# Kernel tuning notes

Measured on AMD Instinct MI355X. Metric: run time of the kernel, lower is better.

## Reference

```python
import jax, jax.numpy as jnp
import numpy as np

V = 50257
VPAD = 50304
D = 768
H = 6
HD = 128
L = 12
T = 2048
BLOCK = 128
NB = T // BLOCK
EPS = 1.1920929e-07  # torch.finfo(float32).eps, F.rms_norm default
ATTN_SCALE = 0.12


def rms_norm(x):
    return x * jax.lax.rsqrt(jnp.mean(jnp.square(x), axis=-1, keepdims=True) + EPS)


def rotary_tables(t):
    af = (1.0 / 1024) ** jnp.linspace(0.0, 1.0, HD // 4)
    af = jnp.concatenate([af, jnp.zeros(HD // 4)])  # half of HD/2 freqs are zero
    theta = jnp.arange(t, dtype=jnp.float32)[:, None] * af[None, :]  # [T, HD/2]
    return jnp.cos(theta), jnp.sin(theta)


def apply_rotary(x, cos, sin):
    # x: [B,T,H,HD]
    x1, x2 = jnp.split(x, 2, axis=-1)
    c = cos[None, :, None, :]
    s = sin[None, :, None, :]
    return jnp.concatenate([x1 * c + x2 * s, -x1 * s + x2 * c], axis=-1)


def build_elem_masks(input_seq, sw_long):
    # Reproduces create_block_masks: block-sparse document-causal + sliding window.
    docs = jnp.cumsum((input_seq == 50256).astype(jnp.int32))
    bi = jnp.arange(NB)
    docs_b = docs.reshape(NB, BLOCK)
    dlo, dhi = docs_b[:, 0], docs_b[:, -1]
    any_bm = (bi[:, None] >= bi[None, :]) & (dlo[:, None] <= dhi[None, :]) & (dhi[:, None] >= dlo[None, :])
    all_bm = (bi[:, None] > bi[None, :]) & (dlo[:, None] == dhi[None, :]) & (dhi[:, None] == dlo[None, :])
    partial_bm = any_bm & (~all_bm)

    def rank_desc(m):
        # rank of each True block among that row's True blocks ordered by descending kv index
        mi = m.astype(jnp.int32)
        return jnp.cumsum(mi[:, ::-1], axis=1)[:, ::-1] - mi

    pr = rank_desc(partial_bm)
    fr = rank_desc(all_bm)
    full_cnt = jnp.sum(all_bm.astype(jnp.int32), axis=1)
    ti = jnp.arange(T)
    causal_e = ti[:, None] >= ti[None, :]
    doc_e = docs[:, None] == docs[None, :]

    def bm(sw):
        # BlockMask.from_kv_blocks keeps nearest blocks:
        # partial kept count = min(partial_cnt, max(sw - full_cnt, 1)); full kept count = min(full_cnt, sw - 1)
        keep_p = partial_bm & (pr < jnp.maximum(sw - full_cnt, 1)[:, None])
        keep_f = all_bm & (fr < (sw - 1))
        kp = jnp.repeat(jnp.repeat(keep_p, BLOCK, axis=0), BLOCK, axis=1)
        kf = jnp.repeat(jnp.repeat(keep_f, BLOCK, axis=0), BLOCK, axis=1)
        # full blocks skip mask_mod; partial blocks apply elementwise document_causal
        return kf | (kp & causal_e & doc_e)

    return bm(sw_long), bm(sw_long // 2)


def attention(x, ve, qkv_w, lam, proj_w, cos, sin, mask):
    B = x.shape[0]
    qkv = jnp.einsum('btd,fd->btf', x, qkv_w.reshape(3 * H * HD, D))
    q, k, v = [a.reshape(B, T, H, HD) for a in jnp.split(qkv, 3, axis=-1)]
    q = apply_rotary(rms_norm(q), cos, sin)
    k = apply_rotary(rms_norm(k), cos, sin)
    if ve is not None:
        v = lam[0] * v + lam[1] * ve.reshape(v.shape)
    else:
        v = lam[0] * v
    scores = jnp.einsum('bthd,bshd->bhts', q, k) * ATTN_SCALE
    scores = jnp.where(mask[None, None], scores, -jnp.inf)
    p = jax.nn.softmax(scores, axis=-1)
    y = jnp.einsum('bhts,bshd->bthd', p, v).reshape(B, T, H * HD)
    return y @ proj_w.T


def mlp(x, fc_w, proj_w):
    h = x @ fc_w.T
    return jnp.square(jax.nn.relu(h)) @ proj_w.T


def forward(input_seq, target_seq, sw, embed_w, ve_w, qkv_w, attn_lambdas, attn_proj_w,
            mlp_fc_w, mlp_proj_w, block_lambdas, skip_weights, lm_head_w):
    long_m, short_m = build_elem_masks(input_seq, sw)
    cos, sin = rotary_tables(T)
    x = x0 = rms_norm(embed_w[input_seq][None])  # [1,T,D]
    ve0, ve1, ve2 = ve_w[0][input_seq], ve_w[1][input_seq], ve_w[2][input_seq]
    ve = [ve0, ve1, ve2, None, None, None, None, None, None, ve0, ve1, ve2]
    enc_masks = [long_m, short_m, short_m, short_m, long_m, short_m]
    masks = enc_masks + enc_masks[::-1]
    skips = []
    for i in range(6):  # encoder
        x = block_lambdas[i, 0] * x + block_lambdas[i, 1] * x0
        x = x + attention(rms_norm(x), ve[i], qkv_w[i], attn_lambdas[i], attn_proj_w[i], cos, sin, masks[i])
        x = x + mlp(rms_norm(x), mlp_fc_w[i], mlp_proj_w[i])
        skips.append(x)
    for j in range(6):  # decoder with U-net skips
        i = 6 + j
        x = x + skip_weights[j] * skips.pop()
        x = block_lambdas[i, 0] * x + block_lambdas[i, 1] * x0
        if i != 7:  # layer 7 has no attention
            x = x + attention(rms_norm(x), ve[i], qkv_w[i], attn_lambdas[i], attn_proj_w[i], cos, sin, masks[i])
        x = x + mlp(rms_norm(x), mlp_fc_w[i], mlp_proj_w[i])
    x = rms_norm(x)
    logits = (x @ lm_head_w.T).astype(jnp.float32)
    logits = 30.0 * jax.nn.sigmoid(logits / (7.5 * (D ** 0.5)))
    logp = jax.nn.log_softmax(logits.reshape(T, VPAD), axis=-1)
    return -jnp.mean(jnp.take_along_axis(logp, target_seq[:, None], axis=1))


def setup_inputs():
    key = jax.random.key(0)
    ks = jax.random.split(key, 10)

    def rn(k, shape, std):
        return jax.random.normal(k, shape, dtype=jnp.float32) * std

    s_d = 0.5 / (D ** 0.5)
    s_h = 0.5 / ((4 * D) ** 0.5)
    input_seq = jax.random.randint(ks[0], (T,), 0, V)
    input_seq = input_seq.at[jnp.arange(0, T, 512)].set(50256)  # doc separators
    return {
        'input_seq': input_seq,
        'target_seq': jax.random.randint(ks[1], (T,), 0, V),
        'sliding_window_num_blocks': 8,
        'embed_w': rn(ks[2], (V, D), 0.02),
        've_w': rn(ks[3], (3, V, D), 0.02),
        'qkv_w': rn(ks[4], (L, 3, H * HD, D), s_d),
        'attn_lambdas': jnp.tile(jnp.array([0.5, 0.5], dtype=jnp.float32), (L, 1)),
        'attn_proj_w': rn(ks[5], (L, D, H * HD), s_d),
        'mlp_fc_w': rn(ks[6], (L, 4 * D, D), s_d),
        'mlp_proj_w': rn(ks[7], (L, D, 4 * D), s_h),
        'block_lambdas': jnp.tile(jnp.array([1.0, 0.0], dtype=jnp.float32), (L, 1)),
        'skip_weights': jnp.ones((6,), dtype=jnp.float32),
        'lm_head_w': rn(ks[8], (VPAD, D), 0.005),
    }


def reference(input_seq, target_seq, sliding_window_num_blocks, embed_w, ve_w, qkv_w,
              attn_lambdas, attn_proj_w, mlp_fc_w, mlp_proj_w, block_lambdas,
              skip_weights, lm_head_w):
    return forward(input_seq, target_seq, sliding_window_num_blocks, embed_w, ve_w, qkv_w,
                   attn_lambdas, attn_proj_w, mlp_fc_w, mlp_proj_w, block_lambdas,
                   skip_weights, lm_head_w)
```

## Files before the change

### kernel.cpp

```cpp
#include <hip/hip_runtime.h>
#include <hip/hip_bf16.h>

#define TT 2048
#define DD 768
#define HH 6
#define HDIM 128
#define NL 12
#define NBL 16
#define BLKSZ 128
#define DFF 3072
#define VP 50304
#define NV 50257
#define EPSF 1.1920929e-07f

typedef unsigned short u16;
typedef __attribute__((ext_vector_type(8))) short short8v;
typedef __attribute__((ext_vector_type(4))) float f32x4;
typedef __attribute__((address_space(3))) void lds_void;
typedef __attribute__((address_space(1))) void gbl_void;

__device__ __forceinline__ u16 f2bf(float f){
  unsigned u = __float_as_uint(f);
  return (u16)((u + 0x7fffu + ((u >> 16) & 1u)) >> 16);
}
__device__ __forceinline__ float bf2f(u16 u){
  return __uint_as_float((unsigned)u << 16);
}
__device__ __forceinline__ void async16(const void* g, void* l){
  __builtin_amdgcn_global_load_lds((const gbl_void*)g, (lds_void*)l, 16, 0, 0);
}

__device__ __forceinline__ float wave_sum(float v){
#pragma unroll
  for (int o = 32; o > 0; o >>= 1) v += __shfl_xor(v, o);
  return v;
}
__device__ __forceinline__ float block_sum(float v){
  __shared__ float sh[9];
  int lane = threadIdx.x & 63, w = threadIdx.x >> 6;
  v = wave_sum(v);
  if (lane == 0) sh[w] = v;
  __syncthreads();
  if (threadIdx.x == 0){
    float tot = 0.f;
    int nw = (blockDim.x + 63) >> 6;
    for (int i = 0; i < nw; i++) tot += sh[i];
    sh[8] = tot;
  }
  __syncthreads();
  return sh[8];
}

__global__ void k_f2bf_all(const float* __restrict__ qkvw, const float* __restrict__ aproj,
                           const float* __restrict__ fcw, const float* __restrict__ mproj,
                           const float* __restrict__ lmw,
                           u16* __restrict__ qkvw_bf, u16* __restrict__ aprojw_bf,
                           u16* __restrict__ fcw_bf, u16* __restrict__ mprojw_bf,
                           u16* __restrict__ lmw_bf){
  const long S0 = 2654208;
  const long S1 = S0 + 884736;
  const long S2 = S1 + 3538944;
  const long S3 = S2 + 3538944;
  const long S4 = S3 + 4829184;
  long stride = (long)gridDim.x * blockDim.x;
  for (long g = (long)blockIdx.x * blockDim.x + threadIdx.x; g < S4; g += stride){
    const float* in; u16* out; long off;
    if (g < S0){ in = qkvw;  out = qkvw_bf;  off = g; }
    else if (g < S1){ in = aproj; out = aprojw_bf; off = g - S0; }
    else if (g < S2){ in = fcw;   out = fcw_bf;   off = g - S1; }
    else if (g < S3){ in = mproj; out = mprojw_bf; off = g - S2; }
    else { in = lmw; out = lmw_bf; off = g - S3; }
    const float4* p = (const float4*)(in + off * 8);
    float4 a = p[0], b = p[1];
    u16 o[8] = { f2bf(a.x), f2bf(a.y), f2bf(a.z), f2bf(a.w),
                 f2bf(b.x), f2bf(b.y), f2bf(b.z), f2bf(b.w) };
    *(ulonglong2*)(out + off * 8) = *(const ulonglong2*)o;
  }
}

__global__ void k_docs_masks(const int* __restrict__ seq, const int* __restrict__ swnb,
                             int* __restrict__ docs, int* __restrict__ bmask){
  if (threadIdx.x != 0) return;
  int c = 0;
  for (int t = 0; t < TT; t++){ c += (seq[t] == 50256); docs[t] = c; }
  int dlo[NBL], dhi[NBL];
  for (int b = 0; b < NBL; b++){ dlo[b] = docs[b*BLKSZ]; dhi[b] = docs[b*BLKSZ + BLKSZ-1]; }
  int allb[NBL][NBL], partb[NBL][NBL];
  for (int i = 0; i < NBL; i++)
    for (int j = 0; j < NBL; j++){
      int a = (i >= j) && (dlo[i] <= dhi[j]) && (dhi[i] >= dlo[j]);
      int f = (i >  j) && (dlo[i] == dhi[j]) && (dhi[i] == dlo[j]);
      allb[i][j] = f; partb[i][j] = a && !f;
    }
  int sws[2]; sws[0] = swnb[0]; sws[1] = swnb[0] / 2;
  for (int m = 0; m < 2; m++){
    int sw = sws[m];
    for (int i = 0; i < NBL; i++){
      int fullcnt = 0;
      for (int j = 0; j < NBL; j++) fullcnt += allb[i][j];
      int pth = sw - fullcnt; if (pth < 1) pth = 1;
      int pr = 0, fr = 0;
      for (int j = NBL-1; j >= 0; j--){
        int kp = partb[i][j] && (pr < pth);
        int kf = allb[i][j]  && (fr < sw - 1);
        bmask[(m*2+0)*NBL*NBL + i*NBL + j] = kf;
        bmask[(m*2+1)*NBL*NBL + i*NBL + j] = kp;
        pr += partb[i][j]; fr += allb[i][j];
      }
    }
  }
}

__global__ void k_embed(const int* __restrict__ seq, const float* __restrict__ embw,
                        const float* __restrict__ vew, float* __restrict__ x,
                        float* __restrict__ x0, u16* __restrict__ veg,
                        float* __restrict__ cosb, float* __restrict__ sinb){
  int t = blockIdx.x;
  if (threadIdx.x < 64){
    int j = threadIdx.x;
    float c = 1.f, s = 0.f;
    if (j < 32){
      float af = powf(1.0f/1024.0f, (float)j / 31.0f);
      float th = (float)t * af;
      c = cosf(th); s = sinf(th);
    }
    cosb[t*64 + j] = c; sinb[t*64 + j] = s;
  }
  int tok = seq[t];
  const float* row = embw + (size_t)tok * DD;
  float ss = 0.f;
  for (int d = threadIdx.x; d < DD; d += blockDim.x){ float v = row[d]; ss += v*v; }
  float tot = block_sum(ss);
  float rn = rsqrtf(tot / DD + EPSF);
  for (int d = threadIdx.x; d < DD; d += blockDim.x){
    float v = row[d] * rn;
    x[(size_t)t*DD + d] = v; x0[(size_t)t*DD + d] = v;
  }
  for (int j = 0; j < 3; j++){
    const float* vr = vew + ((size_t)j*NV + tok) * DD;
    u16* dst = veg + ((size_t)j*TT + t) * DD;
    for (int d = threadIdx.x; d < DD; d += blockDim.x) dst[d] = f2bf(vr[d]);
  }
}

__global__ void k_rmsnorm_bf(const float* __restrict__ in, u16* __restrict__ out,
                             float* __restrict__ rowsum){
  int t = blockIdx.x;
  if (rowsum && threadIdx.x == 0) rowsum[t] = 0.f;
  const float* r = in + (size_t)t * DD;
  float ss = 0.f;
  for (int d = threadIdx.x; d < DD; d += blockDim.x){ float v = r[d]; ss += v*v; }
  float tot = block_sum(ss);
  float rn = rsqrtf(tot / DD + EPSF);
  u16* o = out + (size_t)t * DD;
  for (int d = threadIdx.x; d < DD; d += blockDim.x) o[d] = f2bf(r[d] * rn);
}

__global__ void k_premix_norm(float* __restrict__ x, const float* __restrict__ x0,
                              const float* __restrict__ sk, float* __restrict__ sk_out,
                              const float* __restrict__ skw, int j,
                              const float* __restrict__ bl, int layer, u16* __restrict__ xn){
  int t = blockIdx.x;
  float bl0 = bl[layer*2], bl1 = bl[layer*2 + 1];
  float sw = sk ? skw[j] : 0.f;
  float vloc[3];
  float ss = 0.f;
  int base = t * DD;
#pragma unroll
  for (int k = 0; k < 3; k++){
    int d = threadIdx.x + k*256;
    float xin = x[base + d];
    if (sk_out) sk_out[base + d] = xin;
    float v = xin;
    if (sk) v += sw * sk[base + d];
    v = bl0 * v + bl1 * x0[base + d];
    vloc[k] = v; ss += v*v;
  }
  float tot = block_sum(ss);
  float rn = rsqrtf(tot / DD + EPSF);
#pragma unroll
  for (int k = 0; k < 3; k++){
    int d = threadIdx.x + k*256;
    x[base + d] = vloc[k];
    xn[base + d] = f2bf(vloc[k] * rn);
  }
}

template<int MODE, int BN>
__global__ __launch_bounds__(256, 4) void k_mfma_gemm(const u16* __restrict__ A, const u16* __restrict__ B,
                                                   float* __restrict__ C, u16* __restrict__ Cbf,
                                                   const u16* __restrict__ vegp, const float* __restrict__ lam,
                                                   int layer, u16* __restrict__ vtb,
                                                   int N, int K, int ldk, int nbn){
  constexpr int NW  = BN / 32;
  constexpr int BC  = BN / 64 * 2;
  __shared__ u16 As[128*64];
  __shared__ u16 Bs[BN*64];
  int per = (nbn << 4) >> 3;
  int x = (blockIdx.x & 7) * per + (blockIdx.x >> 3);
  int bm = (x & 15) << 7;
  int bn = (x >> 4) * BN;
  int koff = (MODE == 5) ? blockIdx.y * K : 0;
  int tid = threadIdx.x;
  int wid = tid >> 6, lane = tid & 63;
  int wr = wid >> 1, wc = wid & 1;
  int srow = lane >> 3;
  int scol = (((lane & 7) ^ srow) * 8);
  int l15 = lane & 15, l16 = lane >> 4;
  const u16* pa[4];
  const u16* pb[BC];
#pragma unroll
  for (int c = 0; c < 4; c++){
    int row = (wid*4 + c)*8 + srow;
    pa[c] = A + (size_t)(bm + row) * ldk + koff + scol;
  }
#pragma unroll
  for (int c = 0; c < BC; c++){
    int row = (wid*BC + c)*8 + srow;
    pb[c] = B + (size_t)(bn + row) * ldk + koff + scol;
  }
  f32x4 acc[4][NW] = {};
  for (int k0 = 0; k0 < K; k0 += 64){
#pragma unroll
    for (int c = 0; c < 4; c++){
      async16(pa[c], As + (wid*4 + c) * 512);
      pa[c] += 64;
    }
#pragma unroll
    for (int c = 0; c < BC; c++){
      async16(pb[c], Bs + (wid*BC + c) * 512);
      pb[c] += 64;
    }
    __syncthreads();
#pragma unroll
    for (int kk = 0; kk < 2; kk++){
      short8v a[4], b[NW];
#pragma unroll
      for (int m = 0; m < 4; m++){
        int row = wr*64 + m*16 + l15;
        a[m] = *(const short8v*)(As + row*64 + ((((kk<<2)|l16) ^ (row&7))<<3));
      }
#pragma unroll
      for (int n = 0; n < NW; n++){
        int row = wc*(BN/2) + n*16 + l15;
        b[n] = *(const short8v*)(Bs + row*64 + ((((kk<<2)|l16) ^ (row&7))<<3));
      }
#pragma unroll
      for (int m = 0; m < 4; m++)
#pragma unroll
        for (int n = 0; n < NW; n++)
          acc[m][n] = __builtin_amdgcn_mfma_f32_16x16x32_bf16(a[m], b[n], acc[m][n], 0, 0, 0);
    }
    __syncthreads();
  }
  if (MODE == 4 && bn >= 1536){
    int h = (bn - 1536) >> 7;
    int dbase = (bn - 1536) & 127;
    float l0 = lam[layer*2], l1 = lam[layer*2 + 1];
#pragma unroll
    for (int m = 0; m < 4; m++){
      int t0 = bm + wr*64 + m*16 + l16*4;
#pragma unroll
      for (int n = 0; n < NW; n++){
        int d = dbase + wc*(BN/2) + n*16 + l15;
        u16 o[4];
#pragma unroll
        for (int j = 0; j < 4; j++){
          float v = l0 * acc[m][n][j];
          if (vegp) v += l1 * bf2f(vegp[(size_t)(t0 + j)*DD + h*HDIM + d]);
          o[j] = f2bf(v);
        }
        *(ushort4*)(vtb + ((size_t)(h*HDIM + d))*TT + t0) = *(const ushort4*)o;
      }
    }
    return;
  }
#pragma unroll
  for (int m = 0; m < 4; m++){
    int row = bm + wr*64 + m*16 + l16*4;
#pragma unroll
    for (int j = 0; j < 4; j++){
      if (MODE == 3){
        u16* cb = Cbf + (size_t)(row + j) * N + bn + wc*(BN/2) + l15;
#pragma unroll
        for (int n = 0; n < NW; n++){
          float v = fmaxf(acc[m][n][j], 0.f);
          cb[n*16] = f2bf(v * v);
        }
      } else if (MODE == 4){
        u16* cb = Cbf + (size_t)(row + j) * 1536 + bn + wc*(BN/2) + l15;
#pragma unroll
        for (int n = 0; n < NW; n++) cb[n*16] = f2bf(acc[m][n][j]);
      } else if (MODE == 5){
        float* cp = C + (size_t)(row + j) * N + bn + wc*(BN/2) + l15;
#pragma unroll
        for (int n = 0; n < NW; n++) atomicAdd(cp + n*16, acc[m][n][j]);
      } else {
        float* cp = C + (size_t)(row + j) * N + bn + wc*(BN/2) + l15;
#pragma unroll
        for (int n = 0; n < NW; n++) cp[n*16] = acc[m][n][j];
      }
    }
  }
}

__global__ __launch_bounds__(256) void k_loss_mfma(const u16* __restrict__ A, const u16* __restrict__ B,
                                                   const int* __restrict__ tgt, float* __restrict__ rowsum,
                                                   float* __restrict__ tl){
  __shared__ u16 As[128*64];
  __shared__ u16 Bs[128*64];
  const int nbn = VP/128;
  int per = (nbn << 4) >> 3;
  int x = (blockIdx.x & 7) * per + (blockIdx.x >> 3);
  int bm = (x & 15) << 7;
  int bn = (x >> 4) << 7;
  int tid = threadIdx.x;
  int wid = tid >> 6, lane = tid & 63;
  int wr = wid >> 1, wc = wid & 1;
  int srow = lane >> 3;
  int scol = (((lane & 7) ^ srow) * 8);
  int l15 = lane & 15, l16 = lane >> 4;
  const u16* pa[4];
  const u16* pb[4];
#pragma unroll
  for (int c = 0; c < 4; c++){
    int row = (wid*4 + c)*8 + srow;
    pa[c] = A + (size_t)(bm + row) * DD + scol;
    pb[c] = B + (size_t)(bn + row) * DD + scol;
  }
  f32x4 acc[4][4] = {};
  for (int k0 = 0; k0 < DD; k0 += 64){
#pragma unroll
    for (int c = 0; c < 4; c++){
      int chunk = wid * 4 + c;
      async16(pa[c], As + chunk * 512);
      async16(pb[c], Bs + chunk * 512);
      pa[c] += 64; pb[c] += 64;
    }
    __syncthreads();
#pragma unroll
    for (int kk = 0; kk < 2; kk++){
      short8v a[4], b[4];
#pragma unroll
      for (int m = 0; m < 4; m++)
        a[m] = *(const short8v*)(As + (wr*64 + m*16 + l15)*64 + ((((kk<<2)|l16) ^ (l15&7))<<3));
#pragma unroll
      for (int n = 0; n < 4; n++)
        b[n] = *(const short8v*)(Bs + (wc*64 + n*16 + l15)*64 + ((((kk<<2)|l16) ^ (l15&7))<<3));
#pragma unroll
      for (int m = 0; m < 4; m++)
#pragma unroll
        for (int n = 0; n < 4; n++)
          acc[m][n] = __builtin_amdgcn_mfma_f32_16x16x32_bf16(a[m], b[n], acc[m][n], 0, 0, 0);
    }
    __syncthreads();
  }
  const float INVS = 0.0048112522432469f;
#pragma unroll
  for (int m = 0; m < 4; m++){
#pragma unroll
    for (int j = 0; j < 4; j++){
      int row = bm + wr*64 + m*16 + l16*4 + j;
      int tg = tgt[row];
      float rs = 0.f;
#pragma unroll
      for (int n = 0; n < 4; n++){
        int col = bn + wc*64 + n*16 + l15;
        float lg = 30.f / (1.f + __expf(-acc[m][n][j] * INVS));
        rs += __expf(lg);
        if (col == tg) tl[row] = lg;
      }
      rs += __shfl_xor(rs, 1); rs += __shfl_xor(rs, 2);
      rs += __shfl_xor(rs, 4); rs += __shfl_xor(rs, 8);
      if (l15 == 0) atomicAdd(&rowsum[row], rs);
    }
  }
}

__global__ void k_qkv_post(const u16* __restrict__ qk, const float* __restrict__ cosb,
                           const float* __restrict__ sinb, u16* __restrict__ qbf,
                           u16* __restrict__ kbf){
  int t = blockIdx.x;
  int wv = threadIdx.x >> 6, lane = threadIdx.x & 63;
  float c = cosb[t*64 + lane], s = sinb[t*64 + lane];
  for (int task = wv; task < 12; task += 4){
    int h = task % HH;
    int w = task / HH;
    const u16* p = qk + (size_t)t*1536 + w*768 + h*HDIM;
    float v1 = bf2f(p[lane]), v2 = bf2f(p[lane + 64]);
    float ss = wave_sum(v1*v1 + v2*v2);
    float rn = rsqrtf(ss / 128.f + EPSF);
    v1 *= rn; v2 *= rn;
    float r1 = v1 * c + v2 * s;
    float r2 = -v1 * s + v2 * c;
    u16* dst = (w == 0 ? qbf : kbf) + ((size_t)(h*TT + t))*HDIM;
    dst[lane]      = f2bf(r1);
    dst[lane + 64] = f2bf(r2);
  }
}

__global__ __launch_bounds__(256) void k_attn_mfma(
    const u16* __restrict__ qbf, const u16* __restrict__ kbf, const u16* __restrict__ vtb,
    u16* __restrict__ y, const int* __restrict__ docs,
    const int* __restrict__ kfm, const int* __restrict__ kpm){
  __shared__ u16 Ks[128*128];
  __shared__ u16 Vs[128*128];
  __shared__ int docsL[128];
  __shared__ int kb[NBL], kfl[NBL];
  __shared__ int nkb_sh;
  int wg = (blockIdx.x & 7) * 24 + (blockIdx.x >> 3);
  int h = wg >> 5;
  int qb = (31 - (wg & 31)) * 64;
  int bt = qb >> 7;
  int tid = threadIdx.x;
  int w = tid >> 6, lane = tid & 63;
  int l15 = lane & 15, l16 = lane >> 4;
  if (tid == 0){
    int n = 0;
    for (int sb = 0; sb <= bt; sb++){
      int kf = kfm[bt*NBL + sb], kp = kpm[bt*NBL + sb];
      if (kf || kp){ kb[n] = sb; kfl[n] = kf; n++; }
    }
    nkb_sh = n;
  }
  short8v q[4];
  {
    const u16* qrow = qbf + ((size_t)(h*TT + qb + w*16 + l15))*HDIM;
#pragma unroll
    for (int kc = 0; kc < 4; kc++) q[kc] = *(const short8v*)(qrow + kc*32 + l16*8);
  }
  int t_row[4], dq[4];
#pragma unroll
  for (int j = 0; j < 4; j++){
    t_row[j] = qb + w*16 + l16*4 + j;
    dq[j] = docs[t_row[j]];
  }
  f32x4 o[8] = {};
  float m[4], l[4];
#pragma unroll
  for (int j = 0; j < 4; j++){ m[j] = -1e30f; l[j] = 0.f; }
  __syncthreads();
  int nkb = nkb_sh;
  for (int bi = 0; bi < nkb; bi++){
    int kbi = kb[bi], kf = kfl[bi];
    __syncthreads();
    {
      const u16* ksrc = kbf + ((size_t)(h*TT + kbi*128))*HDIM;
      const u16* vsrc = vtb + ((size_t)(h*HDIM))*TT + kbi*128;
#pragma unroll
      for (int p = 0; p < 8; p++){
        int idx = tid + p*256;
        int r = idx >> 4, c = (idx & 15) * 8;
        short8v kv = *(const short8v*)(ksrc + (size_t)r*HDIM + c);
        *(short8v*)(Ks + ((r*128 + c) ^ ((r&7)<<3))) = kv;
        short8v vv = *(const short8v*)(vsrc + (size_t)r*TT + c);
        *(short8v*)(Vs + ((r*128 + c) ^ ((r&7)<<3))) = vv;
      }
      if (tid < 32) ((int4*)docsL)[tid] = ((const int4*)(docs + kbi*128))[tid];
    }
    __syncthreads();
    f32x4 s[8];
#pragma unroll
    for (int n = 0; n < 8; n++){
      f32x4 acc = {};
#pragma unroll
      for (int kc = 0; kc < 4; kc++){
        int row = n*16 + l15;
        short8v b = *(const short8v*)(Ks + ((row*128 + kc*32 + l16*8) ^ ((row&7)<<3)));
        acc = __builtin_amdgcn_mfma_f32_16x16x32_bf16(q[kc], b, acc, 0, 0, 0);
      }
      s[n] = acc;
    }
    int sbase = kbi*128;
    float bmax[4];
#pragma unroll
    for (int j = 0; j < 4; j++) bmax[j] = -1e30f;
#pragma unroll
    for (int n = 0; n < 8; n++){
      int sg = sbase + n*16 + l15;
      int ds = docsL[n*16 + l15];
#pragma unroll
      for (int j = 0; j < 4; j++){
        float sv = s[n][j] * 0.12f;
        bool keep = kf || ((sg <= t_row[j]) && (ds == dq[j]));
        sv = keep ? sv : -1e30f;
        s[n][j] = sv;
        bmax[j] = fmaxf(bmax[j], sv);
      }
    }
#pragma unroll
    for (int j = 0; j < 4; j++){
#pragma unroll
      for (int off = 1; off < 16; off <<= 1) bmax[j] = fmaxf(bmax[j], __shfl_xor(bmax[j], off));
      float nm = fmaxf(m[j], bmax[j]);
      float r = __expf(m[j] - nm);
      m[j] = nm; l[j] *= r;
#pragma unroll
      for (int n = 0; n < 8; n++) o[n][j] *= r;
    }
    __syncthreads();
#pragma unroll
    for (int n = 0; n < 8; n++){
#pragma unroll
      for (int j = 0; j < 4; j++){
        float sv = s[n][j];
        float p = (sv > -1e29f) ? __expf(sv - m[j]) : 0.f;
        l[j] += p;
        int prow = w*16 + l16*4 + j;
        Ks[((prow*128) + n*16 + l15) ^ ((prow&7)<<3)] = f2bf(p);
      }
    }
    __syncthreads();
    short8v a[4];
    {
      int prow = w*16 + l15;
#pragma unroll
      for (int kc = 0; kc < 4; kc++)
        a[kc] = *(const short8v*)(Ks + ((prow*128 + kc*32 + l16*8) ^ ((prow&7)<<3)));
    }
#pragma unroll
    for (int n = 0; n < 8; n++){
#pragma unroll
      for (int kc = 0; kc < 4; kc++){
        int vrow = n*16 + l15;
        short8v b = *(const short8v*)(Vs + ((vrow*128 + kc*32 + l16*8) ^ ((vrow&7)<<3)));
        o[n] = __builtin_amdgcn_mfma_f32_16x16x32_bf16(a[kc], b, o[n], 0, 0, 0);
      }
    }
  }
  float inv[4];
#pragma unroll
  for (int j = 0; j < 4; j++){
    float lt = l[j];
#pragma unroll
    for (int off = 1; off < 16; off <<= 1) lt += __shfl_xor(lt, off);
    inv[j] = 1.f / lt;
  }
#pragma unroll
  for (int n = 0; n < 8; n++){
#pragma unroll
    for (int j = 0; j < 4; j++)
      y[(size_t)t_row[j]*DD + h*HDIM + n*16 + l15] = f2bf(o[n][j] * inv[j]);
  }
}

__global__ void k_loss_final(const float* __restrict__ rowsum, const float* __restrict__ tl,
                             float* __restrict__ out){
  float a = 0.f;
  for (int t = threadIdx.x; t < TT; t += 256) a += logf(rowsum[t]) - tl[t];
  a = block_sum(a);
  if (threadIdx.x == 0) out[0] = a / TT;
}

extern "C" void kernel_launch(void* const* d_in, const int* in_sizes, int n_in,
                              void* d_out, int out_size, void* d_ws, size_t ws_size,
                              hipStream_t stream){
  const int*   seq   = (const int*)d_in[0];
  const int*   tgt   = (const int*)d_in[1];
  const int*   swnb  = (const int*)d_in[2];
  const float* embw  = (const float*)d_in[3];
  const float* vew   = (const float*)d_in[4];
  const float* qkvw  = (const float*)d_in[5];
  const float* alam  = (const float*)d_in[6];
  const float* aproj = (const float*)d_in[7];
  const float* fcw   = (const float*)d_in[8];
  const float* mproj = (const float*)d_in[9];
  const float* blam  = (const float*)d_in[10];
  const float* skw   = (const float*)d_in[11];
  const float* lmw   = (const float*)d_in[12];

  char* base = (char*)d_ws;
  size_t off = 0;
  auto alloc = [&](size_t bytes){ char* p = base + off; off += (bytes + 255) & ~(size_t)255; return p; };
  float* x     = (float*)alloc((size_t)TT*DD*4);
  float* x0    = (float*)alloc((size_t)TT*DD*4);
  float* skips = (float*)alloc((size_t)5*TT*DD*4);
  float* cosb  = (float*)alloc((size_t)TT*64*4);
  float* sinb  = (float*)alloc((size_t)TT*64*4);
  float* rowsum= (float*)alloc(TT*4);
  float* tl    = (float*)alloc(TT*4);
  int* docs    = (int*)alloc(TT*4);
  int* bmask   = (int*)alloc(4*NBL*NBL*4);
  u16* qk_bf   = (u16*)alloc((size_t)TT*1536*2);
  u16* veg     = (u16*)alloc((size_t)3*TT*DD*2);
  u16* xn_bf   = (u16*)alloc((size_t)TT*DD*2);
  u16* y_bf    = (u16*)alloc((size_t)TT*DD*2);
  u16* hb_bf   = (u16*)alloc((size_t)TT*DFF*2);
  u16* qbf     = (u16*)alloc((size_t)HH*TT*HDIM*2);
  u16* kbf     = (u16*)alloc((size_t)HH*TT*HDIM*2);
  u16* vtb     = (u16*)alloc((size_t)HH*HDIM*TT*2);
  u16* qkvw_bf = (u16*)alloc((size_t)NL*2304*DD*2);
  u16* aprojw_bf = (u16*)alloc((size_t)NL*DD*DD*2);
  u16* fcw_bf  = (u16*)alloc((size_t)NL*DFF*DD*2);
  u16* mprojw_bf = (u16*)alloc((size_t)NL*DD*DFF*2);
  u16* lmw_bf  = (u16*)alloc((size_t)VP*DD*2);

  k_f2bf_all<<<4096, 256, 0, stream>>>(qkvw, aproj, fcw, mproj, lmw,
                                       qkvw_bf, aprojw_bf, fcw_bf, mprojw_bf, lmw_bf);
  k_docs_masks<<<1, 64, 0, stream>>>(seq, swnb, docs, bmask);
  k_embed<<<TT, 256, 0, stream>>>(seq, embw, vew, x, x0, veg, cosb, sinb);

  static const int msel[12] = {0,1,1,1,0,1, 1,0,1,1,1,0};
  for (int i = 0; i < NL; i++){
    const float* sk = nullptr;
    if (i == 6) sk = x;
    else if (i > 6) sk = skips + (size_t)(11 - i)*TT*DD;
    float* sk_out = (i >= 1 && i <= 5) ? (skips + (size_t)(i - 1)*TT*DD) : nullptr;
    k_premix_norm<<<TT, 256, 0, stream>>>(x, x0, sk, sk_out, skw, i - 6, blam, i, xn_bf);
    if (i != 7){
      const u16* vp = nullptr;
      if (i < 3) vp = veg + (size_t)i*TT*DD;
      else if (i >= 9) vp = veg + (size_t)(i - 9)*TT*DD;
      k_mfma_gemm<4,64><<<16*36, 256, 0, stream>>>(xn_bf, qkvw_bf + (size_t)i*2304*DD, nullptr,
                                                   qk_bf, vp, alam, i, vtb, 2304, DD, DD, 36);
      k_qkv_post<<<TT, 256, 0, stream>>>(qk_bf, cosb, sinb, qbf, kbf);
      const int* kfm = bmask + (msel[i]*2 + 0)*NBL*NBL;
      const int* kpm = bmask + (msel[i]*2 + 1)*NBL*NBL;
      k_attn_mfma<<<192, 256, 0, stream>>>(qbf, kbf, vtb, y_bf, docs, kfm, kpm);
      dim3 gap(16*12, 2);
      k_mfma_gemm<5,64><<<gap, 256, 0, stream>>>(y_bf, aprojw_bf + (size_t)i*DD*DD, x,
                                                 nullptr, nullptr, nullptr, 0, nullptr, DD, 384, DD, 12);
      k_rmsnorm_bf<<<TT, 256, 0, stream>>>(x, xn_bf, nullptr);
    }
    k_mfma_gemm<3,64><<<16*48, 256, 0, stream>>>(xn_bf, fcw_bf + (size_t)i*DFF*DD, nullptr,
                                                 hb_bf, nullptr, nullptr, 0, nullptr, DFF, DD, DD, 48);
    dim3 gmp(16*12, 4);
    k_mfma_gemm<5,64><<<gmp, 256, 0, stream>>>(hb_bf, mprojw_bf + (size_t)i*DD*DFF, x,
                                               nullptr, nullptr, nullptr, 0, nullptr, DD, 768, DFF, 12);
  }
  k_rmsnorm_bf<<<TT, 256, 0, stream>>>(x, xn_bf, rowsum);
  k_loss_mfma<<<16*(VP/128), 256, 0, stream>>>(xn_bf, lmw_bf, tgt, rowsum, tl);
  k_loss_final<<<1, 256, 0, stream>>>(rowsum, tl, (float*)d_out);
}
```

Baseline: 2.250 ms.

## Fuse QK rmsnorm and rotary into QKV GEMM epilogue, parallelize doc scan

The QKV projection GEMM now uses 128-wide N tiles so that each tile covers one full head. Its epilogue stages the Q/K tile through shared memory, applies the per-head RMS norm and rotary embedding there, and writes q/k directly. This removes the separate k_qkv_post launch and the round trip of the intermediate bf16 qk buffer. The document-id cumsum is also turned into a 64-lane wave scan instead of a single-thread serial loop. In exchange the QKV GEMM gets larger tiles, half as many blocks, lower occupancy and extra shared memory plus syncs in the epilogue.

Result: faster. 2.179 ms (median of 2 runs) (-3.2%).

```diff
diff --git a/kernel.cpp b/kernel.cpp
--- a/kernel.cpp
+++ b/kernel.cpp
@@ -80,9 +80,23 @@
 
 __global__ void k_docs_masks(const int* __restrict__ seq, const int* __restrict__ swnb,
                              int* __restrict__ docs, int* __restrict__ bmask){
-  if (threadIdx.x != 0) return;
-  int c = 0;
-  for (int t = 0; t < TT; t++){ c += (seq[t] == 50256); docs[t] = c; }
+  int lane = threadIdx.x;
+  int cnt = 0;
+  for (int i = 0; i < 32; i++) cnt += (seq[lane*32 + i] == 50256);
+  int incl = cnt;
+#pragma unroll
+  for (int o = 1; o < 64; o <<= 1){
+    int v = __shfl_up(incl, o);
+    if (lane >= o) incl += v;
+  }
+  int run = incl - cnt;
+  for (int i = 0; i < 32; i++){
+    int t = lane*32 + i;
+    run += (seq[t] == 50256);
+    docs[t] = run;
+  }
+  __syncthreads();
+  if (lane != 0) return;
   int dlo[NBL], dhi[NBL];
   for (int b = 0; b < NBL; b++){ dlo[b] = docs[b*BLKSZ]; dhi[b] = docs[b*BLKSZ + BLKSZ-1]; }
   int allb[NBL][NBL], partb[NBL][NBL];
@@ -187,15 +201,19 @@
 }
 
 template<int MODE, int BN>
-__global__ __launch_bounds__(256, 4) void k_mfma_gemm(const u16* __restrict__ A, const u16* __restrict__ B,
-                                                   float* __restrict__ C, u16* __restrict__ Cbf,
-                                                   const u16* __restrict__ vegp, const float* __restrict__ lam,
-                                                   int layer, u16* __restrict__ vtb,
-                                                   int N, int K, int ldk, int nbn){
+__global__ __launch_bounds__(256, (BN == 64) ? 4 : 2)
+void k_mfma_gemm(const u16* __restrict__ A, const u16* __restrict__ B,
+                 float* __restrict__ C, u16* __restrict__ Cbf,
+                 const u16* __restrict__ vegp, const float* __restrict__ lam,
+                 int layer, u16* __restrict__ vtb,
+                 const float* __restrict__ cosb, const float* __restrict__ sinb,
+                 u16* __restrict__ qbf, u16* __restrict__ kbf,
+                 int N, int K, int ldk, int nbn){
   constexpr int NW  = BN / 32;
   constexpr int BC  = BN / 64 * 2;
   __shared__ u16 As[128*64];
   __shared__ u16 Bs[BN*64];
+  __shared__ float qt[(MODE == 4) ? 32*132 : 1];
   int per = (nbn << 4) >> 3;
   int x = (blockIdx.x & 7) * per + (blockIdx.x >> 3);
   int bm = (x & 15) << 7;
@@ -253,24 +271,72 @@
     }
     __syncthreads();
   }
-  if (MODE == 4 && bn >= 1536){
-    int h = (bn - 1536) >> 7;
-    int dbase = (bn - 1536) & 127;
-    float l0 = lam[layer*2], l1 = lam[layer*2 + 1];
-#pragma unroll
-    for (int m = 0; m < 4; m++){
-      int t0 = bm + wr*64 + m*16 + l16*4;
-#pragma unroll
-      for (int n = 0; n < NW; n++){
-        int d = dbase + wc*(BN/2) + n*16 + l15;
-        u16 o[4];
-#pragma unroll
-        for (int j = 0; j < 4; j++){
-          float v = l0 * acc[m][n][j];
-          if (vegp) v += l1 * bf2f(vegp[(size_t)(t0 + j)*DD + h*HDIM + d]);
-          o[j] = f2bf(v);
+  if (MODE == 4){
+    if (bn >= 1536){
+      int h = (bn - 1536) >> 7;
+      float l0 = lam[layer*2], l1 = lam[layer*2 + 1];
+#pragma unroll
+      for (int m = 0; m < 4; m++){
+        int t0 = bm + wr*64 + m*16 + l16*4;
+#pragma unroll
+        for (int n = 0; n < NW; n++){
+          int d = wc*64 + n*16 + l15;
+          u16 o[4];
+#pragma unroll
+          for (int j = 0; j < 4; j++){
+            float v = l0 * acc[m][n][j];
+            if (vegp) v += l1 * bf2f(vegp[(size_t)(t0 + j)*DD + h*HDIM + d]);
+            o[j] = f2bf(v);
+          }
+          *(ushort4*)(vtb + ((size_t)(h*HDIM + d))*TT + t0) = *(const ushort4*)o;
         }
-        *(ushort4*)(vtb + ((size_t)(h*HDIM + d))*TT + t0) = *(const ushort4*)o;
+      }
+    } else {
+      int h = (bn < 768) ? (bn >> 7) : ((bn - 768) >> 7);
+      u16* dstb = (bn < 768) ? qbf : kbf;
+#pragma unroll
+      for (int p = 0; p < 4; p++){
+        if (wr == (p >> 1)){
+#pragma unroll
+          for (int mm = 0; mm < 2; mm++){
+            int m = (p & 1)*2 + mm;
+#pragma unroll
+            for (int n = 0; n < NW; n++){
+              int col = wc*64 + n*16 + l15;
+#pragma unroll
+              for (int j = 0; j < 4; j++){
+                int lr = m*16 + l16*4 + j - (p & 1)*32;
+                qt[lr*132 + col] = acc[m][n][j];
+              }
+            }
+          }
+        }
+        __syncthreads();
+        {
+          int row = tid >> 3, part = tid & 7;
+          int tok = bm + p*32 + row;
+          float ss = 0.f;
+#pragma unroll
+          for (int jj = 0; jj < 16; jj++){
+            float v = qt[row*132 + part*16 + jj];
+            ss += v*v;
+          }
+          ss += __shfl_xor(ss, 1); ss += __shfl_xor(ss, 2); ss += __shfl_xor(ss, 4);
+          float rn = rsqrtf(ss / 128.f + EPSF);
+          if (part < 4){
+            u16* dst = dstb + ((size_t)(h*TT + tok))*HDIM;
+#pragma unroll
+            for (int jj = 0; jj < 16; jj++){
+              int j = part*16 + jj;
+              float c = cosb[tok*64 + j], s = sinb[tok*64 + j];
+              float v1 = qt[row*132 + j] * rn;
+              float v2 = qt[row*132 + j + 64] * rn;
+              dst[j]      = f2bf(v1*c + v2*s);
+              dst[j + 64] = f2bf(-v1*s + v2*c);
+            }
+          }
+        }
+        __syncthreads();
       }
     }
     return;
@@ -287,10 +353,6 @@
           float v = fmaxf(acc[m][n][j], 0.f);
           cb[n*16] = f2bf(v * v);
         }
-      } else if (MODE == 4){
-        u16* cb = Cbf + (size_t)(row + j) * 1536 + bn + wc*(BN/2) + l15;
-#pragma unroll
-        for (int n = 0; n < NW; n++) cb[n*16] = f2bf(acc[m][n][j]);
       } else if (MODE == 5){
         float* cp = C + (size_t)(row + j) * N + bn + wc*(BN/2) + l15;
 #pragma unroll
@@ -374,28 +436,6 @@
       rs += __shfl_xor(rs, 4); rs += __shfl_xor(rs, 8);
       if (l15 == 0) atomicAdd(&rowsum[row], rs);
     }
-  }
-}
-
-__global__ void k_qkv_post(const u16* __restrict__ qk, const float* __restrict__ cosb,
-                           const float* __restrict__ sinb, u16* __restrict__ qbf,
-                           u16* __restrict__ kbf){
-  int t = blockIdx.x;
-  int wv = threadIdx.x >> 6, lane = threadIdx.x & 63;
-  float c = cosb[t*64 + lane], s = sinb[t*64 + lane];
-  for (int task = wv; task < 12; task += 4){
-    int h = task % HH;
-    int w = task / HH;
-    const u16* p = qk + (size_t)t*1536 + w*768 + h*HDIM;
-    float v1 = bf2f(p[lane]), v2 = bf2f(p[lane + 64]);
-    float ss = wave_sum(v1*v1 + v2*v2);
-    float rn = rsqrtf(ss / 128.f + EPSF);
-    v1 *= rn; v2 *= rn;
-    float r1 = v1 * c + v2 * s;
-    float r2 = -v1 * s + v2 * c;
-    u16* dst = (w == 0 ? qbf : kbf) + ((size_t)(h*TT + t))*HDIM;
-    dst[lane]      = f2bf(r1);
-    dst[lane + 64] = f2bf(r2);
   }
 }
 
@@ -581,7 +621,6 @@
   float* tl    = (float*)alloc(TT*4);
   int* docs    = (int*)alloc(TT*4);
   int* bmask   = (int*)alloc(4*NBL*NBL*4);
-  u16* qk_bf   = (u16*)alloc((size_t)TT*1536*2);
   u16* veg     = (u16*)alloc((size_t)3*TT*DD*2);
   u16* xn_bf   = (u16*)alloc((size_t)TT*DD*2);
   u16* y_bf    = (u16*)alloc((size_t)TT*DD*2);
@@ -611,22 +650,25 @@
       const u16* vp = nullptr;
       if (i < 3) vp = veg + (size_t)i*TT*DD;
       else if (i >= 9) vp = veg + (size_t)(i - 9)*TT*DD;
-      k_mfma_gemm<4,64><<<16*36, 256, 0, stream>>>(xn_bf, qkvw_bf + (size_t)i*2304*DD, nullptr,
-                                                   qk_bf, vp, alam, i, vtb, 2304, DD, DD, 36);
-      k_qkv_post<<<TT, 256, 0, stream>>>(qk_bf, cosb, sinb, qbf, kbf);
+      k_mfma_gemm<4,128><<<16*18, 256, 0, stream>>>(xn_bf, qkvw_bf + (size_t)i*2304*DD, nullptr,
+                                                    nullptr, vp, alam, i, vtb, cosb, sinb, qbf, kbf,
+                                                    2304, DD, DD, 18);
       const int* kfm = bmask + (msel[i]*2 + 0)*NBL*NBL;
       const int* kpm = bmask + (msel[i]*2 + 1)*NBL*NBL;
       k_attn_mfma<<<192, 256, 0, stream>>>(qbf, kbf, vtb, y_bf, docs, kfm, kpm);
       dim3 gap(16*12, 2);
       k_mfma_gemm<5,64><<<gap, 256, 0, stream>>>(y_bf, aprojw_bf + (size_t)i*DD*DD, x,
-                                                 nullptr, nullptr, nullptr, 0, nullptr, DD, 384, DD, 12);
+                                                 nullptr, nullptr, nullptr, 0, nullptr,
+                                                 nullptr, nullptr, nullptr, nullptr, DD, 384, DD, 12);
       k_rmsnorm_bf<<<TT, 256, 0, stream>>>(x, xn_bf, nullptr);
     }
     k_mfma_gemm<3,64><<<16*48, 256, 0, stream>>>(xn_bf, fcw_bf + (size_t)i*DFF*DD, nullptr,
-                                                 hb_bf, nullptr, nullptr, 0, nullptr, DFF, DD, DD, 48);
+                                                 hb_bf, nullptr, nullptr, 0, nullptr,
+                                                 nullptr, nullptr, nullptr, nullptr, DFF, DD, DD, 48);
     dim3 gmp(16*12, 4);
     k_mfma_gemm<5,64><<<gmp, 256, 0, stream>>>(hb_bf, mprojw_bf + (size_t)i*DD*DFF, x,
-                                               nullptr, nullptr, nullptr, 0, nullptr, DD, 768, DFF, 12);
+                                               nullptr, nullptr, nullptr, 0, nullptr,
+                                               nullptr, nullptr, nullptr, nullptr, DD, 768, DFF, 12);
   }
   k_rmsnorm_bf<<<TT, 256, 0, stream>>>(x, xn_bf, rowsum);
   k_loss_mfma<<<16*(VP/128), 256, 0, stream>>>(xn_bf, lmw_bf, tgt, rowsum, tl);
```
